# Kernel tuning notes

Hardware: AMD Instinct MI355X
Metric: run time of the kernel (lower is better)

## Reference

```python
import jax, jax.numpy as jnp
import numpy as np

D = 2048      # d_model
H = 16        # kv_heads
G = 4         # num_groups
HPG = H // G  # heads per group
HD = D // H   # head dim = 128
B, S = 2, 2048


def setup_inputs() -> dict:
    key = jax.random.key(0)
    ks = jax.random.split(key, 5)
    def w(k, shape, fan_in):
        return jax.random.normal(k, shape, jnp.float32) * (fan_in ** -0.5)
    return {
        "x": jax.random.normal(ks[0], (B, S, D), jnp.float32),
        "attn_mask": jnp.ones((S, S), jnp.float32),
        "Wqkv": w(ks[1], (D, 3 * D), D),
        "bqkv": jnp.zeros((3 * D,), jnp.float32),
        "Wq": w(ks[2], (G, HD, HD), HD),   # shared per-group query proj
        "bq": jnp.zeros((G, HD), jnp.float32),
        "Wv": w(ks[3], (G, HD, HD), HD),   # shared per-group value proj
        "bv": jnp.zeros((G, HD), jnp.float32),
    }


def reference(x, attn_mask, Wqkv, bqkv, Wq, bq, Wv, bv):
    Bx, Sx, Dm = x.shape
    qkv = x @ Wqkv + bqkv                      # [B,S,3D]
    q, k, v = jnp.split(qkv, 3, axis=-1)       # each [B,S,D]
    q = q.reshape(Bx, Sx, G, HPG, HD)
    k = k.reshape(Bx, Sx, G, HPG, HD)
    v = v.reshape(Bx, Sx, G, HPG, HD)
    # shared per-group linear applied to every head slice in the group
    q = jnp.einsum('bsghd,gde->bsghe', q, Wq) + bq[None, None, :, None, :]
    v = jnp.einsum('bsghd,gde->bsghe', v, Wv) + bv[None, None, :, None, :]
    scale = HD ** -0.5
    scores = jnp.einsum('bqghd,bkghd->bghqk', q, k) * scale   # [B,G,HPG,S,S]
    attn = jax.nn.softmax(scores, axis=-1)
    attn = attn * attn_mask                    # post-softmax multiplicative mask
    out = jnp.einsum('bghqk,bkghd->bqghd', attn, v)            # [B,S,G,HPG,HD]
    return out.reshape(Bx, Sx, Dm)
```

## Files before the change

kernel.cpp:

```cpp
#include <hip/hip_runtime.h>

typedef __attribute__((ext_vector_type(8))) short short8;
typedef __attribute__((ext_vector_type(4))) float f32x4;
typedef __attribute__((ext_vector_type(4))) unsigned short ushort4v;
typedef unsigned long long u64;

#define DM 2048
#define ND 6144
#define SEQ 2048
#define HD 128
#define QSCALE (0.08838834764831845f * 1.4426950408889634f)

#define MFMA(a, b, c) __builtin_amdgcn_mfma_f32_16x16x32_bf16((a), (b), (c), 0, 0, 0)

__device__ __forceinline__ unsigned short f2bf(float f) {
  unsigned int u = __float_as_uint(f);
  return (unsigned short)((u + 0x7FFFu + ((u >> 16) & 1u)) >> 16);
}
__device__ __forceinline__ float bf2f(unsigned short h) {
  return __uint_as_float(((unsigned int)h) << 16);
}

__global__ void cvt_bf16_kernel(const float* __restrict__ src,
                                unsigned short* __restrict__ dst, int n4) {
  int i = blockIdx.x * blockDim.x + threadIdx.x;
  int st = gridDim.x * blockDim.x;
  for (; i < n4; i += st) {
    f32x4 v = ((const f32x4*)src)[i];
    ushort4v o;
    o[0] = f2bf(v[0]); o[1] = f2bf(v[1]); o[2] = f2bf(v[2]); o[3] = f2bf(v[3]);
    ((ushort4v*)dst)[i] = o;
  }
}

__global__ void transk_kernel(const float* __restrict__ Wqkv,
                              unsigned short* __restrict__ WbT) {
  __shared__ float tile[64 * 68];
  int bx = blockIdx.x;
  int dt = bx >> 5, ct = bx & 31;
  int d0 = dt * 64, c0 = ct * 64;
  int t = threadIdx.x;
#pragma unroll
  for (int j = 0; j < 4; ++j) {
    int el = (t + j * 256) * 4;
    int r = el >> 6, cc = el & 63;
    f32x4 v = *(const f32x4*)(Wqkv + (size_t)(d0 + r) * ND + 2048 + c0 + cc);
    *(f32x4*)(&tile[r * 68 + cc]) = v;
  }
  __syncthreads();
#pragma unroll
  for (int j = 0; j < 4; ++j) {
    int el = (t + j * 256) * 4;
    int c = el >> 6, dd = el & 63;
    ushort4v o;
#pragma unroll
    for (int i = 0; i < 4; ++i) o[i] = f2bf(tile[(dd + i) * 68 + c]);
    *(ushort4v*)(&WbT[(size_t)(2048 + c0 + c) * DM + d0 + dd]) = o;
  }
}

__global__ __launch_bounds__(256) void fold_kernel(const float* __restrict__ Wqkv,
                                                   const float* __restrict__ Wq,
                                                   const float* __restrict__ Wv,
                                                   unsigned short* __restrict__ WbT) {
  __shared__ float wm[128 * 64];
  __shared__ float wt[64 * 128];
  int bx = blockIdx.x;
  int p = bx >> 10;
  int head = (bx >> 6) & 15;
  int dt = (bx >> 1) & 31;
  int eh = bx & 1;
  int g = head >> 2;
  const float* Wm = (p ? Wv : Wq) + g * 16384;
  int cbase = p * 4096 + head * 128;
  int d0 = dt * 64;
  int t = threadIdx.x;
#pragma unroll
  for (int j = 0; j < 8; ++j) {
    int el = (t + j * 256) * 4;
    int dd = el >> 6, e = el & 63;
    *(f32x4*)(&wm[dd * 64 + e]) = *(const f32x4*)(Wm + dd * 128 + eh * 64 + e);
  }
#pragma unroll
  for (int j = 0; j < 8; ++j) {
    int el = (t + j * 256) * 4;
    int r = el >> 7, cc = el & 127;
    *(f32x4*)(&wt[r * 128 + cc]) =
        *(const f32x4*)(Wqkv + (size_t)(d0 + r) * ND + cbase + cc);
  }
  __syncthreads();
  int td = t >> 4, te = t & 15;
  int dl = td * 4, e0 = te * 4;
  float acc[4][4];
#pragma unroll
  for (int i = 0; i < 4; ++i)
#pragma unroll
    for (int j = 0; j < 4; ++j) acc[i][j] = 0.f;
  for (int dd = 0; dd < 128; ++dd) {
    f32x4 bv = *(const f32x4*)(&wm[dd * 64 + e0]);
#pragma unroll
    for (int i = 0; i < 4; ++i) {
      float a = wt[(dl + i) * 128 + dd];
#pragma unroll
      for (int j = 0; j < 4; ++j) acc[i][j] += a * bv[j];
    }
  }
  float sc = p ? 1.0f : QSCALE;
  int outcol0 = p * 4096 + head * 128 + eh * 64 + e0;
#pragma unroll
  for (int j = 0; j < 4; ++j) {
    ushort4v o;
#pragma unroll
    for (int i = 0; i < 4; ++i) o[i] = f2bf(acc[i][j] * sc);
    *(ushort4v*)(&WbT[(size_t)(outcol0 + j) * DM + d0 + dl]) = o;
  }
}

__global__ void bias_kernel(const float* __restrict__ bqkv, const float* __restrict__ Wq,
                            const float* __restrict__ bq, const float* __restrict__ Wv,
                            const float* __restrict__ bv, float* __restrict__ biasf) {
  int col = blockIdx.x * 256 + threadIdx.x;
  if (col >= ND) return;
  float v;
  if (col < 2048) {
    int g = col >> 9, e = col & 127, base = col & ~127;
    float s = 0.f;
    for (int dd = 0; dd < 128; ++dd) s += bqkv[base + dd] * Wq[g * 16384 + dd * 128 + e];
    v = (s + bq[g * 128 + e]) * QSCALE;
  } else if (col < 4096) {
    v = bqkv[col];
  } else {
    int cv = col - 4096;
    int g = cv >> 9, e = cv & 127, base = col & ~127;
    float s = 0.f;
    for (int dd = 0; dd < 128; ++dd) s += bqkv[base + dd] * Wv[g * 16384 + dd * 128 + e];
    v = s + bv[g * 128 + e];
  }
  biasf[col] = v;
}

__global__ __launch_bounds__(512, 2) void gemm_kernel(
    const unsigned short* __restrict__ A, const unsigned short* __restrict__ Bt,
    const float* __restrict__ biasf, unsigned short* __restrict__ Qb,
    unsigned short* __restrict__ Kb, unsigned short* __restrict__ Vt) {
  extern __shared__ char lds[];
  int bid = blockIdx.x;
  int swz = (bid & 7) * 96 + (bid >> 3);
  int bm = swz & 15, bn = swz >> 4;
  int m0 = bm * 256, n0 = bn * 128;
  int tid = threadIdx.x;
  int wid = tid >> 6, lane = tid & 63;
  int ln = lane & 15, hi = lane >> 4;
  int wr = wid >> 1, wc = wid & 1;

  int soff[6];
#pragma unroll
  for (int j = 0; j < 6; ++j) {
    int d = (j < 4 ? j * 8192 : (j - 4) * 8192) + tid * 16;
    int row = d >> 7;
    int p = d ^ ((row & 7) << 4);
    int kof = (p & 127) >> 1;
    soff[j] = (j < 4 ? (m0 + row) : (n0 + row)) * DM + kof;
  }
  auto stage = [&](int buf, int kel) {
#pragma unroll
    for (int j = 0; j < 6; ++j) {
      const unsigned short* s = (j < 4 ? A : Bt) + soff[j] + kel;
      char* dlds = lds + buf * 49152 +
                   (j < 4 ? j * 8192 : 32768 + (j - 4) * 8192) + wid * 1024;
      __builtin_amdgcn_global_load_lds(
          (const __attribute__((address_space(1))) void*)s,
          (__attribute__((address_space(3))) void*)dlds, 16, 0, 0);
    }
  };

  f32x4 acc[4][4] = {};
  const int swzl = (ln & 7) << 4;
  int arow0 = wr * 64 + ln;
  int brow0 = wc * 64 + ln;

  stage(0, 0);
  stage(1, 64);
  asm volatile("s_waitcnt vmcnt(6)" ::: "memory");
  asm volatile("s_barrier" ::: "memory");

  for (int t = 0; t < 32; ++t) {
    char* base = lds + (t & 1) * 49152;
    short8 a0[4], b0[4], a1[4], b1[4];
#pragma unroll
    for (int mi = 0; mi < 4; ++mi)
      a0[mi] = *(const short8*)(base + (((arow0 + mi * 16) * 128 + hi * 16) ^ swzl));
#pragma unroll
    for (int ni = 0; ni < 4; ++ni)
      b0[ni] = *(const short8*)(base + 32768 + (((brow0 + ni * 16) * 128 + hi * 16) ^ swzl));
    __builtin_amdgcn_s_setprio(1);
#pragma unroll
    for (int mi = 0; mi < 4; ++mi)
#pragma unroll
      for (int ni = 0; ni < 4; ++ni)
        acc[mi][ni] = MFMA(a0[mi], b0[ni], acc[mi][ni]);
    __builtin_amdgcn_s_setprio(0);
#pragma unroll
    for (int mi = 0; mi < 4; ++mi)
      a1[mi] = *(const short8*)(base + (((arow0 + mi * 16) * 128 + 64 + hi * 16) ^ swzl));
#pragma unroll
    for (int ni = 0; ni < 4; ++ni)
      b1[ni] = *(const short8*)(base + 32768 + (((brow0 + ni * 16) * 128 + 64 + hi * 16) ^ swzl));
    asm volatile("s_waitcnt lgkmcnt(0)" ::: "memory");
    asm volatile("s_barrier" ::: "memory");
    if (t < 30) stage(t & 1, (t + 2) * 64);
    __builtin_amdgcn_s_setprio(1);
#pragma unroll
    for (int mi = 0; mi < 4; ++mi)
#pragma unroll
      for (int ni = 0; ni < 4; ++ni)
        acc[mi][ni] = MFMA(a1[mi], b1[ni], acc[mi][ni]);
    __builtin_amdgcn_s_setprio(0);
    if (t < 30) {
      asm volatile("s_waitcnt vmcnt(6)" ::: "memory");
    } else if (t == 30) {
      asm volatile("s_waitcnt vmcnt(0)" ::: "memory");
    }
    if (t < 31) asm volatile("s_barrier" ::: "memory");
  }

  int part = n0 >> 11;
  int head = (n0 >> 7) & 15;
  int batch = m0 >> 11;
  int hbuf = batch * 16 + head;
#pragma unroll
  for (int ni = 0; ni < 4; ++ni) {
    int dcol = wc * 64 + ni * 16 + ln;
    float bsv = biasf[n0 + dcol];
#pragma unroll
    for (int mi = 0; mi < 4; ++mi) {
      int srow = (m0 & 2047) + wr * 64 + mi * 16 + hi * 4;
      f32x4 v = acc[mi][ni];
      if (part == 2) {
        ushort4v o = {f2bf(v[0] + bsv), f2bf(v[1] + bsv), f2bf(v[2] + bsv), f2bf(v[3] + bsv)};
        *(ushort4v*)(&Vt[(size_t)(hbuf * 128 + dcol) * SEQ + srow]) = o;
      } else {
        unsigned short* dst = (part ? Kb : Qb) + ((size_t)hbuf * SEQ + srow) * HD + dcol;
        dst[0] = f2bf(v[0] + bsv);
        dst[HD] = f2bf(v[1] + bsv);
        dst[2 * HD] = f2bf(v[2] + bsv);
        dst[3 * HD] = f2bf(v[3] + bsv);
      }
    }
  }
}

__global__ __launch_bounds__(256, 2) void attn_kernel(
    const unsigned short* __restrict__ Qb, const unsigned short* __restrict__ Kb,
    const unsigned short* __restrict__ Vt, const unsigned short* __restrict__ Mb,
    float* __restrict__ out) {
  __shared__ unsigned short Ks[64 * 128];
  __shared__ unsigned short Vs[128 * 64];
  __shared__ unsigned short Ms[128 * 64];
  __shared__ unsigned short Ps[4][32 * 64];
  int bx = blockIdx.x;
  int hb = bx >> 4;
  int q0 = (bx & 15) * 128;
  int b = hb >> 4, head = hb & 15;
  int tid = threadIdx.x, w = tid >> 6, l = tid & 63;
  int ln = l & 15, hi = l >> 4;
  const unsigned short* Qh = Qb + ((size_t)hb * SEQ + q0 + w * 32) * HD;
  const unsigned short* Kh = Kb + (size_t)hb * SEQ * HD;
  const unsigned short* Vh = Vt + (size_t)hb * HD * SEQ;
  char* KsB = (char*)(&Ks[0]);
  char* VsB = (char*)(&Vs[0]);
  char* MsB = (char*)(&Ms[0]);
  char* PwB = (char*)(&Ps[w][0]);

  short8 qf[2][4];
#pragma unroll
  for (int qb = 0; qb < 2; ++qb)
#pragma unroll
    for (int kk = 0; kk < 4; ++kk)
      qf[qb][kk] = *(const short8*)(Qh + (qb * 16 + ln) * HD + kk * 32 + hi * 8);

  f32x4 acc[8][2] = {};
  float mrun[2] = {-1e30f, -1e30f}, Zrun[2] = {0.f, 0.f};

  for (int t = 0; t < 32; ++t) {
    int k0 = t * 64;
    __syncthreads();
    {
      int row = tid >> 2, seg = (tid & 3) * 64;
      const unsigned short* src = Kh + (size_t)(k0 + row) * HD + (seg >> 1);
      short8 tv[4];
#pragma unroll
      for (int j = 0; j < 4; ++j) tv[j] = *(const short8*)(src + j * 8);
#pragma unroll
      for (int j = 0; j < 4; ++j)
        *(short8*)(KsB + ((row * 256 + seg + j * 16) ^ ((row & 7) << 4))) = tv[j];
    }
    {
      int row = tid >> 1, seg = (tid & 1) * 64;
      const unsigned short* src = Vh + (size_t)row * SEQ + k0 + (seg >> 1);
      short8 tv[4];
#pragma unroll
      for (int j = 0; j < 4; ++j) tv[j] = *(const short8*)(src + j * 8);
#pragma unroll
      for (int j = 0; j < 4; ++j)
        *(short8*)(VsB + ((row * 128 + seg + j * 16) ^ ((row & 7) << 4))) = tv[j];
    }
    {
      int row = tid >> 1, seg = (tid & 1) * 64;
      const unsigned short* src = Mb + (size_t)(q0 + row) * SEQ + k0 + (seg >> 1);
      short8 tv[4];
#pragma unroll
      for (int j = 0; j < 4; ++j) tv[j] = *(const short8*)(src + j * 8);
#pragma unroll
      for (int j = 0; j < 4; ++j)
        *(short8*)(MsB + ((row * 128 + seg + j * 16) ^ ((row & 7) << 4))) = tv[j];
    }
    __syncthreads();

    f32x4 sAcc[4][2] = {};
#pragma unroll
    for (int kk = 0; kk < 4; ++kk) {
#pragma unroll
      for (int mb = 0; mb < 4; ++mb) {
        int key = mb * 16 + ln;
        short8 kf = *(const short8*)(KsB + ((key * 256 + kk * 64 + hi * 16) ^ ((key & 7) << 4)));
        sAcc[mb][0] = MFMA(kf, qf[0][kk], sAcc[mb][0]);
        sAcc[mb][1] = MFMA(kf, qf[1][kk], sAcc[mb][1]);
      }
    }

#pragma unroll
    for (int qb = 0; qb < 2; ++qb) {
      float tm = -1e30f;
#pragma unroll
      for (int mb = 0; mb < 4; ++mb)
#pragma unroll
        for (int r = 0; r < 4; ++r) tm = fmaxf(tm, sAcc[mb][qb][r]);
      tm = fmaxf(tm, __shfl_xor(tm, 16));
      tm = fmaxf(tm, __shfl_xor(tm, 32));
      float mn = fmaxf(mrun[qb], tm);
      float al = __builtin_amdgcn_exp2f(mrun[qb] - mn);
      mrun[qb] = mn;
      float ts = 0.f;
      int qrow = w * 32 + qb * 16 + ln;
      int swzm = (qrow & 7) << 4;
      int swzp = (ln & 7) << 4;
#pragma unroll
      for (int mb = 0; mb < 4; ++mb) {
        u64 mk = *(const u64*)(MsB + ((qrow * 128 + mb * 32 + hi * 8) ^ swzm));
        u64 pk = 0;
#pragma unroll
        for (int r = 0; r < 4; ++r) {
          float p = __builtin_amdgcn_exp2f(sAcc[mb][qb][r] - mn);
          ts += p;
          float pm = p * bf2f((unsigned short)(mk >> (16 * r)));
          pk |= ((u64)f2bf(pm)) << (16 * r);
        }
        *(u64*)(PwB + (((qb * 16 + ln) * 128 + mb * 32 + hi * 8) ^ swzp)) = pk;
      }
      ts += __shfl_xor(ts, 16);
      ts += __shfl_xor(ts, 32);
      Zrun[qb] = Zrun[qb] * al + ts;
#pragma unroll
      for (int db = 0; db < 8; ++db) acc[db][qb] *= al;
    }

#pragma unroll
    for (int kv = 0; kv < 2; ++kv) {
      short8 pf[2];
#pragma unroll
      for (int qb = 0; qb < 2; ++qb)
        pf[qb] = *(const short8*)(PwB + (((qb * 16 + ln) * 128 + kv * 64 + hi * 16) ^ ((ln & 7) << 4)));
#pragma unroll
      for (int db = 0; db < 8; ++db) {
        int d = db * 16 + ln;
        short8 vf = *(const short8*)(VsB + ((d * 128 + kv * 64 + hi * 16) ^ ((d & 7) << 4)));
        acc[db][0] = MFMA(vf, pf[0], acc[db][0]);
        acc[db][1] = MFMA(vf, pf[1], acc[db][1]);
      }
    }
  }

#pragma unroll
  for (int qb = 0; qb < 2; ++qb) {
    float rz = 1.0f / Zrun[qb];
    int srow = q0 + w * 32 + qb * 16 + ln;
    float* dst = out + ((size_t)(b * SEQ + srow)) * DM + head * HD + hi * 4;
#pragma unroll
    for (int db = 0; db < 8; ++db) {
      f32x4 o;
#pragma unroll
      for (int r = 0; r < 4; ++r) o[r] = acc[db][qb][r] * rz;
      *(f32x4*)(dst + db * 16) = o;
    }
  }
}

extern "C" void kernel_launch(void* const* d_in, const int* in_sizes, int n_in,
                              void* d_out, int out_size, void* d_ws, size_t ws_size,
                              hipStream_t stream) {
  (void)in_sizes; (void)n_in; (void)out_size; (void)ws_size;
  const float* x    = (const float*)d_in[0];
  const float* mask = (const float*)d_in[1];
  const float* Wqkv = (const float*)d_in[2];
  const float* bqkv = (const float*)d_in[3];
  const float* Wq   = (const float*)d_in[4];
  const float* bq   = (const float*)d_in[5];
  const float* Wv   = (const float*)d_in[6];
  const float* bv   = (const float*)d_in[7];
  float* out = (float*)d_out;
  char* ws = (char*)d_ws;

  unsigned short* xb    = (unsigned short*)(ws);
  unsigned short* maskb = (unsigned short*)(ws + 16777216);
  unsigned short* WbT   = (unsigned short*)(ws + 25165824);
  float*          biasf = (float*)(ws + 50331648);
  unsigned short* Qb    = (unsigned short*)(ws + 50356224);
  unsigned short* Kb    = (unsigned short*)(ws + 67133440);
  unsigned short* Vt    = (unsigned short*)(ws + 83910656);

  hipFuncSetAttribute((const void*)gemm_kernel,
                      hipFuncAttributeMaxDynamicSharedMemorySize, 98304);

  cvt_bf16_kernel<<<2048, 256, 0, stream>>>(x, xb, 2097152);
  cvt_bf16_kernel<<<1024, 256, 0, stream>>>(mask, maskb, 1048576);
  transk_kernel<<<1024, 256, 0, stream>>>(Wqkv, WbT);
  fold_kernel<<<2048, 256, 0, stream>>>(Wqkv, Wq, Wv, WbT);
  bias_kernel<<<24, 256, 0, stream>>>(bqkv, Wq, bq, Wv, bv, biasf);
  gemm_kernel<<<768, 512, 98304, stream>>>(xb, WbT, biasf, Qb, Kb, Vt);
  attn_kernel<<<512, 256, 0, stream>>>(Qb, Kb, Vt, maskb, out);
}
```

Before: 430.9 us.

## Prefetch next KV/mask tile into registers and lazily rescale softmax state

Global loads for the next K, V and mask tile are issued into registers before the compute of the current tile, so global latency overlaps with the MFMA and softmax work. Barriers become raw s_waitcnt/s_barrier. The online-softmax rescale of the accumulator and running sum is skipped unless some lane's tile max exceeds the running max by more than 8 (log2 units), which removes the per-tile multiply over 16 accumulator vectors. Risks are higher register pressure from the prefetch buffers and larger unnormalized exponentials, bounded by 2^8.

```diff
diff --git a/kernel.cpp b/kernel.cpp
--- a/kernel.cpp
+++ b/kernel.cpp
@@ -272,6 +272,22 @@
   char* MsB = (char*)(&Ms[0]);
   char* PwB = (char*)(&Ps[w][0]);
 
+  int krow = tid >> 2, kseg = (tid & 3) * 64;
+  int vrow = tid >> 1, vseg = (tid & 1) * 64;
+  const unsigned short* Kst = Kh + (size_t)krow * HD + (kseg >> 1);
+  const unsigned short* Vst = Vh + (size_t)vrow * SEQ + (vseg >> 1);
+  const unsigned short* Mst = Mb + (size_t)(q0 + vrow) * SEQ + (vseg >> 1);
+
+  short8 kq[4], vq[4], mq[4];
+  auto issue = [&](int k0) {
+#pragma unroll
+    for (int j = 0; j < 4; ++j) kq[j] = *(const short8*)(Kst + (size_t)k0 * HD + j * 8);
+#pragma unroll
+    for (int j = 0; j < 4; ++j) vq[j] = *(const short8*)(Vst + k0 + j * 8);
+#pragma unroll
+    for (int j = 0; j < 4; ++j) mq[j] = *(const short8*)(Mst + k0 + j * 8);
+  };
+
   short8 qf[2][4];
 #pragma unroll
   for (int qb = 0; qb < 2; ++qb)
@@ -282,40 +298,23 @@
   f32x4 acc[8][2] = {};
   float mrun[2] = {-1e30f, -1e30f}, Zrun[2] = {0.f, 0.f};
 
+  issue(0);
   for (int t = 0; t < 32; ++t) {
     int k0 = t * 64;
-    __syncthreads();
-    {
-      int row = tid >> 2, seg = (tid & 3) * 64;
-      const unsigned short* src = Kh + (size_t)(k0 + row) * HD + (seg >> 1);
-      short8 tv[4];
-#pragma unroll
-      for (int j = 0; j < 4; ++j) tv[j] = *(const short8*)(src + j * 8);
-#pragma unroll
-      for (int j = 0; j < 4; ++j)
-        *(short8*)(KsB + ((row * 256 + seg + j * 16) ^ ((row & 7) << 4))) = tv[j];
-    }
-    {
-      int row = tid >> 1, seg = (tid & 1) * 64;
-      const unsigned short* src = Vh + (size_t)row * SEQ + k0 + (seg >> 1);
-      short8 tv[4];
-#pragma unroll
-      for (int j = 0; j < 4; ++j) tv[j] = *(const short8*)(src + j * 8);
-#pragma unroll
-      for (int j = 0; j < 4; ++j)
-        *(short8*)(VsB + ((row * 128 + seg + j * 16) ^ ((row & 7) << 4))) = tv[j];
-    }
-    {
-      int row = tid >> 1, seg = (tid & 1) * 64;
-      const unsigned short* src = Mb + (size_t)(q0 + row) * SEQ + k0 + (seg >> 1);
-      short8 tv[4];
-#pragma unroll
-      for (int j = 0; j < 4; ++j) tv[j] = *(const short8*)(src + j * 8);
-#pragma unroll
-      for (int j = 0; j < 4; ++j)
-        *(short8*)(MsB + ((row * 128 + seg + j * 16) ^ ((row & 7) << 4))) = tv[j];
-    }
-    __syncthreads();
+    asm volatile("s_waitcnt lgkmcnt(0)" ::: "memory");
+    asm volatile("s_barrier" ::: "memory");
+#pragma unroll
+    for (int j = 0; j < 4; ++j)
+      *(short8*)(KsB + ((krow * 256 + kseg + j * 16) ^ ((krow & 7) << 4))) = kq[j];
+#pragma unroll
+    for (int j = 0; j < 4; ++j)
+      *(short8*)(VsB + ((vrow * 128 + vseg + j * 16) ^ ((vrow & 7) << 4))) = vq[j];
+#pragma unroll
+    for (int j = 0; j < 4; ++j)
+      *(short8*)(MsB + ((vrow * 128 + vseg + j * 16) ^ ((vrow & 7) << 4))) = mq[j];
+    if (t < 31) issue(k0 + 64);
+    asm volatile("s_waitcnt lgkmcnt(0)" ::: "memory");
+    asm volatile("s_barrier" ::: "memory");
 
     f32x4 sAcc[4][2] = {};
 #pragma unroll
@@ -338,10 +337,15 @@
         for (int r = 0; r < 4; ++r) tm = fmaxf(tm, sAcc[mb][qb][r]);
       tm = fmaxf(tm, __shfl_xor(tm, 16));
       tm = fmaxf(tm, __shfl_xor(tm, 32));
-      float mn = fmaxf(mrun[qb], tm);
-      float al = __builtin_amdgcn_exp2f(mrun[qb] - mn);
-      mrun[qb] = mn;
-      float ts = 0.f;
+      if (!__all((tm - mrun[qb]) <= 8.0f)) {
+        float mn = fmaxf(mrun[qb], tm);
+        float al = __builtin_amdgcn_exp2f(mrun[qb] - mn);
+        mrun[qb] = mn;
+        Zrun[qb] *= al;
+#pragma unroll
+        for (int db = 0; db < 8; ++db) acc[db][qb] *= al;
+      }
+      float ts0 = 0.f, ts1 = 0.f, ts2 = 0.f, ts3 = 0.f;
       int qrow = w * 32 + qb * 16 + ln;
       int swzm = (qrow & 7) << 4;
       int swzp = (ln & 7) << 4;
@@ -349,20 +353,21 @@
       for (int mb = 0; mb < 4; ++mb) {
         u64 mk = *(const u64*)(MsB + ((qrow * 128 + mb * 32 + hi * 8) ^ swzm));
         u64 pk = 0;
-#pragma unroll
-        for (int r = 0; r < 4; ++r) {
-          float p = __builtin_amdgcn_exp2f(sAcc[mb][qb][r] - mn);
-          ts += p;
-          float pm = p * bf2f((unsigned short)(mk >> (16 * r)));
-          pk |= ((u64)f2bf(pm)) << (16 * r);
-        }
+        float p0 = __builtin_amdgcn_exp2f(sAcc[mb][qb][0] - mrun[qb]);
+        float p1 = __builtin_amdgcn_exp2f(sAcc[mb][qb][1] - mrun[qb]);
+        float p2 = __builtin_amdgcn_exp2f(sAcc[mb][qb][2] - mrun[qb]);
+        float p3 = __builtin_amdgcn_exp2f(sAcc[mb][qb][3] - mrun[qb]);
+        ts0 += p0; ts1 += p1; ts2 += p2; ts3 += p3;
+        pk |= ((u64)f2bf(p0 * bf2f((unsigned short)(mk))));
+        pk |= ((u64)f2bf(p1 * bf2f((unsigned short)(mk >> 16)))) << 16;
+        pk |= ((u64)f2bf(p2 * bf2f((unsigned short)(mk >> 32)))) << 32;
+        pk |= ((u64)f2bf(p3 * bf2f((unsigned short)(mk >> 48)))) << 48;
         *(u64*)(PwB + (((qb * 16 + ln) * 128 + mb * 32 + hi * 8) ^ swzp)) = pk;
       }
+      float ts = (ts0 + ts1) + (ts2 + ts3);
       ts += __shfl_xor(ts, 16);
       ts += __shfl_xor(ts, 32);
-      Zrun[qb] = Zrun[qb] * al + ts;
-#pragma unroll
-      for (int db = 0; db < 8; ++db) acc[db][qb] *= al;
+      Zrun[qb] += ts;
     }
 
 #pragma unroll
```

New measurement: 470.9 us. 9.3% more time.
